# Optimization experiments

Measured on AMD Instinct MI355X. Metric: run time of the kernel, lower is better.

Reference implementation:

```python
import jax, jax.numpy as jnp
import numpy as np

E = 512
H = 8
D = E // H
WIN = 128  # mask_window_size


def setup_inputs() -> dict:
    key = jax.random.key(0)
    k1, k2, k3, k4, k5 = jax.random.split(key, 5)
    B, L = 2, 4096
    s = 1.0 / np.sqrt(E)
    return {
        "x": jax.random.normal(k1, (B, L, E), dtype=jnp.float32),
        "in_proj_w": jax.random.normal(k2, (3 * E, E), dtype=jnp.float32) * s,
        "in_proj_b": jax.random.normal(k3, (3 * E,), dtype=jnp.float32) * 0.02,
        "out_w": jax.random.normal(k4, (E, E), dtype=jnp.float32) * s,
        "out_b": jax.random.normal(k5, (E,), dtype=jnp.float32) * 0.02,
    }


def reference(x, in_proj_w, in_proj_b, out_w, out_b):
    B, L, _ = x.shape
    # fused qkv projection (torch MultiheadAttention in_proj): x @ W.T + b
    qkv = jnp.einsum("ble,fe->blf", x, in_proj_w) + in_proj_b  # [B,L,3E]
    q, k, v = jnp.split(qkv, 3, axis=-1)
    # [B,H,L,D]
    q = q.reshape(B, L, H, D).transpose(0, 2, 1, 3)
    k = k.reshape(B, L, H, D).transpose(0, 2, 1, 3)
    v = v.reshape(B, L, H, D).transpose(0, 2, 1, 3)
    scores = jnp.einsum("bhqd,bhkd->bhqk", q, k) / jnp.sqrt(jnp.float32(D))
    # (diagonal stays blocked — faithful to the original gen_mask quirk)
    idx = jnp.arange(L)
    dist = jnp.abs(idx[:, None] - idx[None, :])
    blocked = (dist > WIN) | (dist == 0)  # [L,L]
    scores = jnp.where(blocked[None, None], -jnp.inf, scores)
    attn = jax.nn.softmax(scores, axis=-1)  # [B,H,L,L]
    out = jnp.einsum("bhqk,bhkd->bhqd", attn, v)  # [B,H,L,D]
    out = out.transpose(0, 2, 1, 3).reshape(B, L, E)
    return jnp.einsum("ble,fe->blf", out, out_w) + out_b
```

## Files before the change

kernel.cpp:

```cpp
#include <hip/hip_runtime.h>
#include <math.h>

#define E_DIM 512
#define H_DIM 8
#define WIN 128
#define L_SEQ 4096
#define B_SZ 2

typedef unsigned short ushort_t;
typedef unsigned int uint_t;
typedef __attribute__((ext_vector_type(8))) __bf16 bf16x8;
typedef __attribute__((ext_vector_type(4))) float f32x4;

__device__ __forceinline__ ushort_t f2bf(float f) {
    uint_t u = __float_as_uint(f);
    u = u + 0x7fffu + ((u >> 16) & 1u);
    return (ushort_t)(u >> 16);
}
__device__ __forceinline__ float bf2f(ushort_t h) {
    return __uint_as_float((uint_t)h << 16);
}

__device__ __forceinline__ void gload16(const ushort_t* g, ushort_t* l) {
    __builtin_amdgcn_global_load_lds(
        (const __attribute__((address_space(1))) void*)g,
        (__attribute__((address_space(3))) void*)l,
        16, 0, 0);
}


__global__ __launch_bounds__(256) void convertX(
    const float* __restrict__ x,  ushort_t* __restrict__ xh,
    const float* __restrict__ w1, ushort_t* __restrict__ w1h,
    const float* __restrict__ w2, ushort_t* __restrict__ w2h) {
    int sg = blockIdx.x * 256 + threadIdx.x;
    const float* src; ushort_t* dh;
    if (sg < 524288)      { src = x;  dh = xh; }
    else if (sg < 622592) { src = w1; dh = w1h; sg -= 524288; }
    else                  { src = w2; dh = w2h; sg -= 622592; }
    const int tile = sg >> 6, slot = sg & 63;
    const int row = (tile >> 4) * 16 + (slot & 15);
    const int k   = (tile & 15) * 32 + (slot >> 4) * 8;
    const float4 v0 = *(const float4*)&src[(size_t)row * 512 + k];
    const float4 v1 = *(const float4*)&src[(size_t)row * 512 + k + 4];
    const float vv[8] = {v0.x, v0.y, v0.z, v0.w, v1.x, v1.y, v1.z, v1.w};
    union { ushort_t u[8]; ushort4 v[2]; } h;
    #pragma unroll
    for (int j = 0; j < 8; j++) h.u[j] = f2bf(vv[j]);
    ((ushort4*)(dh + (size_t)sg * 8))[0] = h.v[0];
    ((ushort4*)(dh + (size_t)sg * 8))[1] = h.v[1];
}

__global__ __launch_bounds__(256) void gemm_qkv(
    const ushort_t* __restrict__ Ah,
    const ushort_t* __restrict__ Wh,
    const float* __restrict__ bias,
    ushort_t* __restrict__ qTh,
    ushort_t* __restrict__ kTh,
    ushort_t* __restrict__ vTh) {
    __shared__ __align__(16) ushort_t sAh[2][8 * 512];
    __shared__ __align__(16) ushort_t sWh[2][8 * 512];

    const int tid = threadIdx.x, lane = tid & 63, w = tid >> 6;
    const int wm = w & 1, wn = w >> 1, ln = lane & 15, quad = lane >> 4;
    const int bx = blockIdx.x, by = blockIdx.y;
    const int lo8 = lane * 8;
    const int wu = __builtin_amdgcn_readfirstlane(w);

    f32x4 acc[4][4];
    const f32x4 zero = {0.f, 0.f, 0.f, 0.f};
    #pragma unroll
    for (int i = 0; i < 4; i++)
        #pragma unroll
        for (int j = 0; j < 4; j++) acc[i][j] = zero;

    const ushort_t* pb[4];
    ushort_t* db0[4];
    ushort_t* db1[4];
    #pragma unroll
    for (int t = 0; t < 4; t++) {
        const int g = wu * 4 + t;
        if (g < 8) {
            pb[t] = Ah + ((size_t)(bx * 8 + g) * 16) * 512;
            db0[t] = &sAh[0][g * 512]; db1[t] = &sAh[1][g * 512];
        } else {
            const int u = g - 8;
            pb[t] = Wh + ((size_t)(by * 8 + u) * 16) * 512;
            db0[t] = &sWh[0][u * 512]; db1[t] = &sWh[1][u * 512];
        }
    }

    #pragma unroll
    for (int t = 0; t < 4; t++)
        gload16(pb[t] + lo8, db0[t]);

    for (int kt = 0; kt < 16; kt++) {
        __syncthreads();
        if (kt < 15) {
            const int koff = (kt + 1) * 512;
            if ((kt + 1) & 1) {
                #pragma unroll
                for (int t = 0; t < 4; t++) gload16(pb[t] + koff + lo8, db1[t]);
            } else {
                #pragma unroll
                for (int t = 0; t < 4; t++) gload16(pb[t] + koff + lo8, db0[t]);
            }
        }
        const int cb = kt & 1;
        bf16x8 fah[4];
        #pragma unroll
        for (int i = 0; i < 4; i++)
            fah[i] = *(const bf16x8*)&sAh[cb][(wm * 4 + i) * 512 + lo8];
        #pragma unroll
        for (int j = 0; j < 4; j++) {
            const bf16x8 fbh = *(const bf16x8*)&sWh[cb][(wn * 4 + j) * 512 + lo8];
            #pragma unroll
            for (int i = 0; i < 4; i++)
                acc[i][j] = __builtin_amdgcn_mfma_f32_16x16x32_bf16(fah[i], fbh, acc[i][j], 0, 0, 0);
        }
    }

    const int b = bx >> 5;
    const int h = 2 * (by & 3) + wn;
    if (by < 8) {
        ushort_t* dh = (by < 4) ? qTh : kTh;
        #pragma unroll
        for (int i = 0; i < 4; i++) {
            const int rt = (bx & 31) * 8 + wm * 4 + i;
            const size_t tb = ((size_t)(b * 8 + h) * 256 + rt) * 2;
            #pragma unroll
            for (int j = 0; j < 4; j++) {
                const float bv = bias[by * 128 + wn * 64 + j * 16 + ln];
                const size_t tile = tb + (j >> 1);
                #pragma unroll
                for (int r = 0; r < 4; r++) {
                    const int slot = ((j * 2 + (ln >> 3)) & 3) * 16 + quad * 4 + r;
                    const size_t idx = tile * 512 + slot * 8 + (ln & 7);
                    dh[idx] = f2bf(acc[i][j][r] + bv);
                }
            }
        }
    } else {
        const int kwin = (bx & 31) * 2 + wm;
        #pragma unroll
        for (int i = 0; i < 4; i++) {
            const int kk = i >> 1;
            #pragma unroll
            for (int j = 0; j < 4; j++) {
                const float bv = bias[by * 128 + wn * 64 + j * 16 + ln];
                const size_t tile = (((size_t)(b * 8 + h) * 64 + kwin) * 4 + j) * 2 + kk;
                #pragma unroll
                for (int r = 0; r < 4; r++) {
                    const int klq = quad * 4 + r;
                    const int slot = ((i & 1) * 2 + (klq >> 3)) * 16 + ln;
                    const size_t idx = tile * 512 + slot * 8 + (klq & 7);
                    vTh[idx] = f2bf(acc[i][j][r] + bv);
                }
            }
        }
    }
}

__global__ __launch_bounds__(512) void attn_mfma(
    const ushort_t* __restrict__ qTh,
    const ushort_t* __restrict__ kTh,
    const ushort_t* __restrict__ vTh,
    ushort_t* __restrict__ outh) {
    __shared__ __align__(16) ushort_t sKh[2][8 * 512];
    __shared__ __align__(16) ushort_t sV [2][8 * 512];
    __shared__ __align__(16) ushort_t sP [16 * 512];

    const int qs = blockIdx.x * 128;
    const int h = blockIdx.y, b = blockIdx.z;
    const int bh = b * 8 + h;
    const int tid = threadIdx.x, lane = tid & 63;
    const int w = tid >> 6, ln = lane & 15, quad = lane >> 4;
    const int lo8 = lane * 8;

    bf16x8 qf[2];
    {
        const size_t qt = ((size_t)bh * 256 + (qs >> 4) + w) * 2;
        qf[0] = *(const bf16x8*)(qTh + (qt + 0) * 512 + lo8);
        qf[1] = *(const bf16x8*)(qTh + (qt + 1) * 512 + lo8);
    }

    f32x4 oacc[4];
    const f32x4 zero = {0.f, 0.f, 0.f, 0.f};
    #pragma unroll
    for (int dt = 0; dt < 4; dt++) oacc[dt] = zero;
    float m_run[4], l_run[4];
    #pragma unroll
    for (int r = 0; r < 4; r++) { m_run[r] = -1e30f; l_run[r] = 0.f; }

    const float cscale = 0.125f * 1.44269504f;
    const int qlo = qs + 16 * w;

    {
        if (w < 4) {
            int st = (qs >> 4) - 8 + w;
            st = st < 0 ? 0 : (st > 255 ? 255 : st);
            const size_t kb = ((size_t)bh * 256 + st) * 2 * 512 + lo8;
            gload16(kTh + kb,       &sKh[0][(w * 2 + 0) * 512]);
            gload16(kTh + kb + 512, &sKh[0][(w * 2 + 1) * 512]);
        } else {
            const int u = w - 4;
            int vw = (qs >> 6) - 2;
            vw = vw < 0 ? 0 : (vw > 63 ? 63 : vw);
            const size_t vb = (((size_t)bh * 64 + vw) * 4 + u) * 2 * 512 + lo8;
            gload16(vTh + vb,       &sV[0][(u * 2 + 0) * 512]);
            gload16(vTh + vb + 512, &sV[0][(u * 2 + 1) * 512]);
        }
    }

    for (int kt = 0; kt < 6; kt++) {
        const int ks = qs - 128 + kt * 64;

        __syncthreads();

        if (kt < 5) {
            const int nb = (kt + 1) & 1;
            if (w < 4) {
                int st = (qs >> 4) - 8 + (kt + 1) * 4 + w;
                st = st < 0 ? 0 : (st > 255 ? 255 : st);
                const size_t kb = ((size_t)bh * 256 + st) * 2 * 512 + lo8;
                gload16(kTh + kb,       &sKh[nb][(w * 2 + 0) * 512]);
                gload16(kTh + kb + 512, &sKh[nb][(w * 2 + 1) * 512]);
            } else {
                const int u = w - 4;
                int vw = (qs >> 6) - 2 + kt + 1;
                vw = vw < 0 ? 0 : (vw > 63 ? 63 : vw);
                const size_t vb = (((size_t)bh * 64 + vw) * 4 + u) * 2 * 512 + lo8;
                gload16(vTh + vb,       &sV[nb][(u * 2 + 0) * 512]);
                gload16(vTh + vb + 512, &sV[nb][(u * 2 + 1) * 512]);
            }
        }
        const int cb = kt & 1;

        f32x4 sacc[4];
        #pragma unroll
        for (int jt = 0; jt < 4; jt++) {
            f32x4 a = zero;
            const int klo = ks + 16 * jt;
            const bool dead = (klo > qlo + 15 + WIN) || (klo + 15 < qlo - WIN) ||
                              (klo >= L_SEQ) || (klo + 15 < 0);
            if (!dead) {
                #pragma unroll
                for (int kk = 0; kk < 2; kk++) {
                    const bf16x8 kh = *(const bf16x8*)&sKh[cb][(jt * 2 + kk) * 512 + lo8];
                    a = __builtin_amdgcn_mfma_f32_16x16x32_bf16(qf[kk], kh, a, 0, 0, 0);
                }
            }
            sacc[jt] = a;
        }

        float u[4][4];
        #pragma unroll
        for (int jt = 0; jt < 4; jt++) {
            const int kcol = ks + 16 * jt + ln;
            #pragma unroll
            for (int r = 0; r < 4; r++) {
                const int qrow = qlo + quad * 4 + r;
                const int dist = qrow > kcol ? qrow - kcol : kcol - qrow;
                const bool ok = (kcol >= 0) && (kcol < L_SEQ) && (dist >= 1) && (dist <= WIN);
                u[jt][r] = ok ? sacc[jt][r] * cscale : -INFINITY;
            }
        }
        float mk[4];
        #pragma unroll
        for (int r = 0; r < 4; r++)
            mk[r] = fmaxf(fmaxf(u[0][r], u[1][r]), fmaxf(u[2][r], u[3][r]));
        #pragma unroll
        for (int off = 1; off <= 8; off <<= 1)
            #pragma unroll
            for (int r = 0; r < 4; r++)
                mk[r] = fmaxf(mk[r], __shfl_xor(mk[r], off));

        float alpha[4], psum[4], p[4][4];
        #pragma unroll
        for (int r = 0; r < 4; r++) {
            const float mnew = fmaxf(fmaxf(m_run[r], mk[r]), -1e30f);
            alpha[r] = exp2f(m_run[r] - mnew);
            m_run[r] = mnew;
            psum[r] = 0.f;
            #pragma unroll
            for (int jt = 0; jt < 4; jt++) {
                p[jt][r] = exp2f(u[jt][r] - mnew);
                psum[r] += p[jt][r];
            }
        }
        #pragma unroll
        for (int off = 1; off <= 8; off <<= 1)
            #pragma unroll
            for (int r = 0; r < 4; r++)
                psum[r] += __shfl_xor(psum[r], off);
        #pragma unroll
        for (int r = 0; r < 4; r++)
            l_run[r] = l_run[r] * alpha[r] + psum[r];

        #pragma unroll
        for (int dt = 0; dt < 4; dt++)
            #pragma unroll
            for (int r = 0; r < 4; r++)
                oacc[dt][r] *= alpha[r];

        #pragma unroll
        for (int jt = 0; jt < 4; jt++)
            #pragma unroll
            for (int r = 0; r < 4; r++) {
                const int slot = ((jt & 1) * 2 + (ln >> 3)) * 16 + quad * 4 + r;
                sP[w * 1024 + (jt >> 1) * 512 + slot * 8 + (ln & 7)] = f2bf(p[jt][r]);
            }

        #pragma unroll
        for (int kk = 0; kk < 2; kk++) {
            const bf16x8 pf = *(const bf16x8*)&sP[w * 1024 + kk * 512 + lo8];
            #pragma unroll
            for (int dt = 0; dt < 4; dt++) {
                const bf16x8 vf = *(const bf16x8*)&sV[cb][(dt * 2 + kk) * 512 + lo8];
                oacc[dt] = __builtin_amdgcn_mfma_f32_16x16x32_bf16(pf, vf, oacc[dt], 0, 0, 0);
            }
        }
    }

    const int Rt = ((b * L_SEQ + qs) >> 4) + w;
    #pragma unroll
    for (int r = 0; r < 4; r++) {
        const float inv_l = 1.f / l_run[r];
        #pragma unroll
        for (int dt = 0; dt < 4; dt++) {
            const float v = oacc[dt][r] * inv_l;
            const int tile = Rt * 16 + h * 2 + (dt >> 1);
            const int slot = ((dt & 1) * 2 + (ln >> 3)) * 16 + quad * 4 + r;
            const size_t idx = (size_t)tile * 512 + slot * 8 + (ln & 7);
            outh[idx] = f2bf(v);
        }
    }
}

__global__ __launch_bounds__(512) void gemm_out(
    const ushort_t* __restrict__ Ah,
    const ushort_t* __restrict__ Wh,
    const float* __restrict__ bias, float* __restrict__ C) {
    __shared__ __align__(16) ushort_t sAh[2][16 * 512];
    __shared__ __align__(16) ushort_t sWh[2][8 * 512];

    const int tid = threadIdx.x, lane = tid & 63, w = tid >> 6;
    const int wm = w & 3, wn = w >> 2, ln = lane & 15, quad = lane >> 4;
    const int bx = blockIdx.x, by = blockIdx.y;
    const int lo8 = lane * 8;
    const int wu = __builtin_amdgcn_readfirstlane(w);

    f32x4 acc[2][2];
    const f32x4 zero = {0.f, 0.f, 0.f, 0.f};
    #pragma unroll
    for (int i = 0; i < 2; i++)
        #pragma unroll
        for (int j = 0; j < 2; j++) acc[i][j] = zero;

    const ushort_t* pb[3];
    ushort_t* db0[3];
    ushort_t* db1[3];
    #pragma unroll
    for (int t = 0; t < 3; t++) {
        const int g = wu * 3 + t;
        if (g < 16) {
            pb[t] = Ah + ((size_t)(bx * 8 + (g >> 1)) * 16 + (g & 1)) * 512;
            db0[t] = &sAh[0][g * 512]; db1[t] = &sAh[1][g * 512];
        } else {
            const int u = g - 16;
            pb[t] = Wh + ((size_t)(by * 4 + (u >> 1)) * 16 + (u & 1)) * 512;
            db0[t] = &sWh[0][u * 512]; db1[t] = &sWh[1][u * 512];
        }
    }

    #pragma unroll
    for (int t = 0; t < 3; t++)
        gload16(pb[t] + lo8, db0[t]);

    for (int KT = 0; KT < 8; KT++) {
        __syncthreads();
        if (KT < 7) {
            const int koff = (KT + 1) * 1024;
            if ((KT + 1) & 1) {
                #pragma unroll
                for (int t = 0; t < 3; t++) gload16(pb[t] + koff + lo8, db1[t]);
            } else {
                #pragma unroll
                for (int t = 0; t < 3; t++) gload16(pb[t] + koff + lo8, db0[t]);
            }
        }
        const int cb = KT & 1;
        #pragma unroll
        for (int ks = 0; ks < 2; ks++) {
            bf16x8 fah[2];
            #pragma unroll
            for (int i = 0; i < 2; i++)
                fah[i] = *(const bf16x8*)&sAh[cb][((wm * 2 + i) * 2 + ks) * 512 + lo8];
            #pragma unroll
            for (int j = 0; j < 2; j++) {
                const bf16x8 fbh = *(const bf16x8*)&sWh[cb][((wn * 2 + j) * 2 + ks) * 512 + lo8];
                #pragma unroll
                for (int i = 0; i < 2; i++)
                    acc[i][j] = __builtin_amdgcn_mfma_f32_16x16x32_bf16(fah[i], fbh, acc[i][j], 0, 0, 0);
            }
        }
    }

    #pragma unroll
    for (int i = 0; i < 2; i++) {
        const int row0 = bx * 128 + wm * 32 + i * 16 + quad * 4;
        #pragma unroll
        for (int j = 0; j < 2; j++) {
            const int col = by * 64 + wn * 32 + j * 16 + ln;
            const float bv = bias[col];
            #pragma unroll
            for (int r = 0; r < 4; r++)
                C[(size_t)(row0 + r) * E_DIM + col] = acc[i][j][r] + bv;
        }
    }
}

extern "C" void kernel_launch(void* const* d_in, const int* in_sizes, int n_in,
                              void* d_out, int out_size, void* d_ws, size_t ws_size,
                              hipStream_t stream) {
    const float* x         = (const float*)d_in[0];
    const float* in_proj_w = (const float*)d_in[1];
    const float* in_proj_b = (const float*)d_in[2];
    const float* out_w     = (const float*)d_in[3];
    const float* out_b     = (const float*)d_in[4];
    float* out = (float*)d_out;

    const int N = B_SZ * L_SEQ;
    const size_t NE = (size_t)N * E_DIM;

    char* p = (char*)d_ws;
    ushort_t* xh  = (ushort_t*)p; p += NE * 2;
    ushort_t* w1h = (ushort_t*)p; p += (size_t)3 * E_DIM * E_DIM * 2;
    ushort_t* w2h = (ushort_t*)p; p += (size_t)E_DIM * E_DIM * 2;
    ushort_t* qTh = (ushort_t*)p; p += NE * 2;
    ushort_t* kTh = (ushort_t*)p; p += NE * 2;
    ushort_t* vTh = (ushort_t*)p; p += NE * 2;
    ushort_t* ath = (ushort_t*)p; p += NE * 2;

    convertX<<<2560, 256, 0, stream>>>(x, xh, in_proj_w, w1h, out_w, w2h);

    gemm_qkv<<<dim3(64, 12), 256, 0, stream>>>(
        xh, w1h, in_proj_b, qTh, kTh, vTh);

    attn_mfma<<<dim3(L_SEQ / 128, H_DIM, B_SZ), 512, 0, stream>>>(
        qTh, kTh, vTh, ath);

    gemm_out<<<dim3(64, 8), 512, 0, stream>>>(
        ath, w2h, out_b, out);
}
```

Measured before the change: 136.4 us.

## Transpose QK^T MFMA so softmax stats are per-lane, skip dead key tiles

The QK^T MFMA operands are swapped so each lane owns one query row, which turns the row max and row sum reductions into two cross-quad shuffles instead of four shuffle rounds over four rows. Softmax work is skipped for key subtiles that lie entirely outside the window, and a whole key iteration is skipped when every subtile is dead. The P tile is written to LDS with packed ushort4 stores. Alpha and l are broadcast back to the accumulator layout with __shfl, which adds a few shuffles, and masked tiles now write explicit zeros.

After: 130.4 us. 1.05x faster.

```diff
diff --git a/kernel.cpp b/kernel.cpp
--- a/kernel.cpp
+++ b/kernel.cpp
@@ -188,12 +188,11 @@
     const f32x4 zero = {0.f, 0.f, 0.f, 0.f};
     #pragma unroll
     for (int dt = 0; dt < 4; dt++) oacc[dt] = zero;
-    float m_run[4], l_run[4];
-    #pragma unroll
-    for (int r = 0; r < 4; r++) { m_run[r] = -1e30f; l_run[r] = 0.f; }
+    float m_run = -1e30f, l_run = 0.f;
 
     const float cscale = 0.125f * 1.44269504f;
     const int qlo = qs + 16 * w;
+    const int q = qlo + ln;
 
     {
         if (w < 4) {
@@ -236,88 +235,100 @@
         }
         const int cb = kt & 1;
 
-        f32x4 sacc[4];
+        bool dead[4];
         #pragma unroll
         for (int jt = 0; jt < 4; jt++) {
-            f32x4 a = zero;
             const int klo = ks + 16 * jt;
-            const bool dead = (klo > qlo + 15 + WIN) || (klo + 15 < qlo - WIN) ||
-                              (klo >= L_SEQ) || (klo + 15 < 0);
-            if (!dead) {
-                #pragma unroll
-                for (int kk = 0; kk < 2; kk++) {
-                    const bf16x8 kh = *(const bf16x8*)&sKh[cb][(jt * 2 + kk) * 512 + lo8];
-                    a = __builtin_amdgcn_mfma_f32_16x16x32_bf16(qf[kk], kh, a, 0, 0, 0);
-                }
-            }
-            sacc[jt] = a;
-        }
-
-        float u[4][4];
-        #pragma unroll
-        for (int jt = 0; jt < 4; jt++) {
-            const int kcol = ks + 16 * jt + ln;
-            #pragma unroll
-            for (int r = 0; r < 4; r++) {
-                const int qrow = qlo + quad * 4 + r;
-                const int dist = qrow > kcol ? qrow - kcol : kcol - qrow;
-                const bool ok = (kcol >= 0) && (kcol < L_SEQ) && (dist >= 1) && (dist <= WIN);
-                u[jt][r] = ok ? sacc[jt][r] * cscale : -INFINITY;
-            }
-        }
-        float mk[4];
-        #pragma unroll
-        for (int r = 0; r < 4; r++)
-            mk[r] = fmaxf(fmaxf(u[0][r], u[1][r]), fmaxf(u[2][r], u[3][r]));
-        #pragma unroll
-        for (int off = 1; off <= 8; off <<= 1)
+            dead[jt] = (klo > qlo + 15 + WIN) || (klo + 15 < qlo - WIN) ||
+                       (klo >= L_SEQ) || (klo + 15 < 0);
+        }
+        const bool ktAlive = !(dead[0] && dead[1] && dead[2] && dead[3]);
+
+        if (ktAlive) {
+            f32x4 st4[4];
+            #pragma unroll
+            for (int jt = 0; jt < 4; jt++) {
+                f32x4 a = zero;
+                if (!dead[jt]) {
+                    #pragma unroll
+                    for (int kk = 0; kk < 2; kk++) {
+                        const bf16x8 kh = *(const bf16x8*)&sKh[cb][(jt * 2 + kk) * 512 + lo8];
+                        a = __builtin_amdgcn_mfma_f32_16x16x32_bf16(kh, qf[kk], a, 0, 0, 0);
+                    }
+                }
+                st4[jt] = a;
+            }
+
+            float uv[4][4];
+            float mk = -INFINITY;
+            #pragma unroll
+            for (int jt = 0; jt < 4; jt++) {
+                if (!dead[jt]) {
+                    #pragma unroll
+                    for (int r = 0; r < 4; r++) {
+                        const int kcol = ks + jt * 16 + quad * 4 + r;
+                        const int dist = q > kcol ? q - kcol : kcol - q;
+                        const bool ok = (kcol >= 0) && (kcol < L_SEQ) && (dist >= 1) && (dist <= WIN);
+                        const float val = ok ? st4[jt][r] * cscale : -INFINITY;
+                        uv[jt][r] = val;
+                        mk = fmaxf(mk, val);
+                    }
+                }
+            }
+            mk = fmaxf(mk, __shfl_xor(mk, 16));
+            mk = fmaxf(mk, __shfl_xor(mk, 32));
+
+            const float mnew = fmaxf(m_run, mk);
+            const float alpha = exp2f(m_run - mnew);
+            m_run = mnew;
+
+            float ps = 0.f;
+            #pragma unroll
+            for (int jt = 0; jt < 4; jt++) {
+                if (!dead[jt]) {
+                    #pragma unroll
+                    for (int r = 0; r < 4; r++) {
+                        const float pv = exp2f(uv[jt][r] - mnew);
+                        uv[jt][r] = pv;
+                        ps += pv;
+                    }
+                }
+            }
+            ps += __shfl_xor(ps, 16);
+            ps += __shfl_xor(ps, 32);
+            l_run = l_run * alpha + ps;
+
+            float ar[4];
             #pragma unroll
             for (int r = 0; r < 4; r++)
-                mk[r] = fmaxf(mk[r], __shfl_xor(mk[r], off));
-
-        float alpha[4], psum[4], p[4][4];
-        #pragma unroll
-        for (int r = 0; r < 4; r++) {
-            const float mnew = fmaxf(fmaxf(m_run[r], mk[r]), -1e30f);
-            alpha[r] = exp2f(m_run[r] - mnew);
-            m_run[r] = mnew;
-            psum[r] = 0.f;
+                ar[r] = __shfl(alpha, quad * 4 + r);
+            #pragma unroll
+            for (int dt = 0; dt < 4; dt++)
+                #pragma unroll
+                for (int r = 0; r < 4; r++)
+                    oacc[dt][r] *= ar[r];
+
             #pragma unroll
             for (int jt = 0; jt < 4; jt++) {
-                p[jt][r] = exp2f(u[jt][r] - mnew);
-                psum[r] += p[jt][r];
-            }
-        }
-        #pragma unroll
-        for (int off = 1; off <= 8; off <<= 1)
-            #pragma unroll
-            for (int r = 0; r < 4; r++)
-                psum[r] += __shfl_xor(psum[r], off);
-        #pragma unroll
-        for (int r = 0; r < 4; r++)
-            l_run[r] = l_run[r] * alpha[r] + psum[r];
-
-        #pragma unroll
-        for (int dt = 0; dt < 4; dt++)
-            #pragma unroll
-            for (int r = 0; r < 4; r++)
-                oacc[dt][r] *= alpha[r];
-
-        #pragma unroll
-        for (int jt = 0; jt < 4; jt++)
-            #pragma unroll
-            for (int r = 0; r < 4; r++) {
-                const int slot = ((jt & 1) * 2 + (ln >> 3)) * 16 + quad * 4 + r;
-                sP[w * 1024 + (jt >> 1) * 512 + slot * 8 + (ln & 7)] = f2bf(p[jt][r]);
-            }
-
-        #pragma unroll
-        for (int kk = 0; kk < 2; kk++) {
-            const bf16x8 pf = *(const bf16x8*)&sP[w * 1024 + kk * 512 + lo8];
-            #pragma unroll
-            for (int dt = 0; dt < 4; dt++) {
-                const bf16x8 vf = *(const bf16x8*)&sV[cb][(dt * 2 + kk) * 512 + lo8];
-                oacc[dt] = __builtin_amdgcn_mfma_f32_16x16x32_bf16(pf, vf, oacc[dt], 0, 0, 0);
+                ushort4 pw;
+                if (!dead[jt]) {
+                    pw.x = f2bf(uv[jt][0]); pw.y = f2bf(uv[jt][1]);
+                    pw.z = f2bf(uv[jt][2]); pw.w = f2bf(uv[jt][3]);
+                } else {
+                    pw.x = 0; pw.y = 0; pw.z = 0; pw.w = 0;
+                }
+                const int slot = ((jt & 1) * 2 + (quad >> 1)) * 16 + ln;
+                *(ushort4*)&sP[w * 1024 + (jt >> 1) * 512 + slot * 8 + (quad & 1) * 4] = pw;
+            }
+
+            #pragma unroll
+            for (int kk = 0; kk < 2; kk++) {
+                const bf16x8 pf = *(const bf16x8*)&sP[w * 1024 + kk * 512 + lo8];
+                #pragma unroll
+                for (int dt = 0; dt < 4; dt++) {
+                    const bf16x8 vf = *(const bf16x8*)&sV[cb][(dt * 2 + kk) * 512 + lo8];
+                    oacc[dt] = __builtin_amdgcn_mfma_f32_16x16x32_bf16(pf, vf, oacc[dt], 0, 0, 0);
+                }
             }
         }
     }
@@ -325,7 +336,8 @@
     const int Rt = ((b * L_SEQ + qs) >> 4) + w;
     #pragma unroll
     for (int r = 0; r < 4; r++) {
-        const float inv_l = 1.f / l_run[r];
+        const float lr = __shfl(l_run, quad * 4 + r);
+        const float inv_l = 1.f / lr;
         #pragma unroll
         for (int dt = 0; dt < 4; dt++) {
             const float v = oacc[dt][r] * inv_l;
```
